# Performance work log

Hardware: AMD Instinct MI355X
Metric: run time of the kernel (lower is better)

The kernel has to match this reference:

```python
import jax, jax.numpy as jnp
import numpy as np

D = 2048  # input_size
H = 2048  # hidden_size
K = 4096  # number of children


def setup_inputs() -> dict:
    key = jax.random.key(0)
    ks = jax.random.split(key, 12)
    sD = 1.0 / np.sqrt(D)
    sH = 1.0 / np.sqrt(H)
    return {
        "input": jax.random.normal(ks[0], (D,), dtype=jnp.float32),
        "children_c": jax.random.normal(ks[1], (K, H), dtype=jnp.float32),
        "children_h": jax.random.normal(ks[2], (K, H), dtype=jnp.float32),
        "W_iou_x": jax.random.uniform(ks[3], (3 * H, D), jnp.float32, -sD, sD),
        "b_iou_x": jax.random.uniform(ks[4], (3 * H,), jnp.float32, -sD, sD),
        "W_iou_h": jax.random.uniform(ks[5], (3 * H, H), jnp.float32, -sH, sH),
        "b_iou_h": jax.random.uniform(ks[6], (3 * H,), jnp.float32, -sH, sH),
        "W_fx": jax.random.uniform(ks[7], (H, D), jnp.float32, -sD, sD),
        "b_fx": jax.random.uniform(ks[8], (H,), jnp.float32, -sD, sD),
        "W_fh": jax.random.uniform(ks[9], (H, H), jnp.float32, -sH, sH),
        "b_fh": jax.random.uniform(ks[10], (H,), jnp.float32, -sH, sH),
    }


def reference(input, children_c, children_h,
              W_iou_x, b_iou_x, W_iou_h, b_iou_h,
              W_fx, b_fx, W_fh, b_fh):
    # iou = iou_x(input) + iou_h(sum_k h_k)  -> [3H]
    h_sum = jnp.sum(children_h, axis=0)
    iou = (W_iou_x @ input + b_iou_x) + (W_iou_h @ h_sum + b_iou_h)
    i, o, u = jnp.split(iou, 3)
    i = jax.nn.sigmoid(i)
    o = jax.nn.sigmoid(o)
    u = jnp.tanh(u)
    # per-child forget gates, batched over K (original loops in Python):
    # f_k = sigmoid(f_x(input) + f_h(h_k))  -> [K, H]
    fx = W_fx @ input + b_fx                       # [H], computed once
    fh = children_h @ W_fh.T + b_fh                # [K, H] GEMM
    f = jax.nn.sigmoid(fx[None, :] + fh)           # [K, H]
    c = i * u + jnp.sum(f * children_c, axis=0)    # [H]
    h = o * jnp.tanh(c)                            # [H]
    return (o, c, h)
```

## Files before the change

### kernel.cpp

```cpp
#include <hip/hip_runtime.h>

typedef unsigned short u16;
typedef short bf16x8 __attribute__((ext_vector_type(8)));
typedef float f32x4 __attribute__((ext_vector_type(4)));

#define D_IN 2048
#define H_DIM 2048
#define K_CH 4096

__device__ __forceinline__ u16 f2bf(float f) {
  unsigned int u = __float_as_uint(f);
  u += 0x7fffu + ((u >> 16) & 1u);
  return (u16)(u >> 16);
}
__device__ __forceinline__ float sigmoidf(float x) {
  return 1.0f / (1.0f + __expf(-x));
}
__device__ __forceinline__ uint4 packrow(float4 a, float4 b) {
  uint4 w;
  w.x = (unsigned)f2bf(a.x) | ((unsigned)f2bf(a.y) << 16);
  w.y = (unsigned)f2bf(a.z) | ((unsigned)f2bf(a.w) << 16);
  w.z = (unsigned)f2bf(b.x) | ((unsigned)f2bf(b.y) << 16);
  w.w = (unsigned)f2bf(b.z) | ((unsigned)f2bf(b.w) << 16);
  return w;
}

__global__ __launch_bounds__(256) void kprep(const float* __restrict__ ch,
                                             const float* __restrict__ wfh,
                                             float* __restrict__ partials,
                                             u16* __restrict__ chb,
                                             u16* __restrict__ wfhb) {
  const int t = threadIdx.x;
  if (blockIdx.x < 256) {
    const int r0 = blockIdx.x * 16;
    float s0 = 0.f, s1 = 0.f, s2 = 0.f, s3 = 0.f;
    float s4 = 0.f, s5 = 0.f, s6 = 0.f, s7 = 0.f;
#pragma unroll
    for (int gq = 0; gq < 4; ++gq) {
      float4 a[4], b[4];
#pragma unroll
      for (int r = 0; r < 4; ++r) {
        const float4* p =
            (const float4*)(ch + (size_t)(r0 + gq * 4 + r) * H_DIM + t * 8);
        a[r] = p[0];
        b[r] = p[1];
      }
#pragma unroll
      for (int r = 0; r < 4; ++r) {
        s0 += a[r].x; s1 += a[r].y; s2 += a[r].z; s3 += a[r].w;
        s4 += b[r].x; s5 += b[r].y; s6 += b[r].z; s7 += b[r].w;
        *(uint4*)(chb + (size_t)(r0 + gq * 4 + r) * H_DIM + t * 8) =
            packrow(a[r], b[r]);
      }
    }
    float4 lo, hi;
    lo.x = s0; lo.y = s1; lo.z = s2; lo.w = s3;
    hi.x = s4; hi.y = s5; hi.z = s6; hi.w = s7;
    float* pp = partials + (size_t)blockIdx.x * H_DIM + t * 8;
    *(float4*)pp = lo;
    *(float4*)(pp + 4) = hi;
  } else {
    const size_t base = (size_t)(blockIdx.x - 256) * 16384 + t * 8;
#pragma unroll
    for (int gq = 0; gq < 2; ++gq) {
      float4 a[4], b[4];
#pragma unroll
      for (int j = 0; j < 4; ++j) {
        const float4* p = (const float4*)(wfh + base + (gq * 4 + j) * 2048);
        a[j] = p[0];
        b[j] = p[1];
      }
#pragma unroll
      for (int j = 0; j < 4; ++j)
        *(uint4*)(wfhb + base + (gq * 4 + j) * 2048) = packrow(a[j], b[j]);
    }
  }
}

__global__ __launch_bounds__(256) void kred(const float* __restrict__ partials,
                                            float* __restrict__ hsum) {
  const int c = blockIdx.x * 256 + threadIdx.x;
  float acc0 = 0.f, acc1 = 0.f, acc2 = 0.f, acc3 = 0.f;
  float acc4 = 0.f, acc5 = 0.f, acc6 = 0.f, acc7 = 0.f;
  for (int p = 0; p < 256; p += 8) {
    acc0 += partials[(size_t)(p + 0) * H_DIM + c];
    acc1 += partials[(size_t)(p + 1) * H_DIM + c];
    acc2 += partials[(size_t)(p + 2) * H_DIM + c];
    acc3 += partials[(size_t)(p + 3) * H_DIM + c];
    acc4 += partials[(size_t)(p + 4) * H_DIM + c];
    acc5 += partials[(size_t)(p + 5) * H_DIM + c];
    acc6 += partials[(size_t)(p + 6) * H_DIM + c];
    acc7 += partials[(size_t)(p + 7) * H_DIM + c];
  }
  hsum[c] = ((acc0 + acc1) + (acc2 + acc3)) + ((acc4 + acc5) + (acc6 + acc7));
}

__global__ __launch_bounds__(256) void kmatvec(
    const float* __restrict__ Wix, const float* __restrict__ bix,
    const float* __restrict__ Wih, const float* __restrict__ bih,
    const float* __restrict__ Wfx, const float* __restrict__ bfx,
    const float* __restrict__ bfh, const float* __restrict__ x,
    const float* __restrict__ hsum, float* __restrict__ iou,
    float* __restrict__ g) {
  const int wave = threadIdx.x >> 6, lane = threadIdx.x & 63;
  const int row = blockIdx.x * 4 + wave;
  float s = 0.f;
  if (row < 6144) {
    const float4* wx = (const float4*)(Wix + (size_t)row * D_IN);
    const float4* wh = (const float4*)(Wih + (size_t)row * H_DIM);
    const float4* xv = (const float4*)x;
    const float4* hv = (const float4*)hsum;
#pragma unroll
    for (int i = 0; i < 8; ++i) {
      int idx = i * 64 + lane;
      float4 a = wx[idx], b = xv[idx];
      s += a.x * b.x + a.y * b.y + a.z * b.z + a.w * b.w;
      float4 c = wh[idx], d = hv[idx];
      s += c.x * d.x + c.y * d.y + c.z * d.z + c.w * d.w;
    }
#pragma unroll
    for (int off = 32; off > 0; off >>= 1) s += __shfl_xor(s, off);
    if (lane == 0) iou[row] = s + bix[row] + bih[row];
  } else {
    const int h = row - 6144;
    const float4* w = (const float4*)(Wfx + (size_t)h * D_IN);
    const float4* xv = (const float4*)x;
#pragma unroll
    for (int i = 0; i < 8; ++i) {
      int idx = i * 64 + lane;
      float4 a = w[idx], b = xv[idx];
      s += a.x * b.x + a.y * b.y + a.z * b.z + a.w * b.w;
    }
#pragma unroll
    for (int off = 32; off > 0; off >>= 1) s += __shfl_xor(s, off);
    if (lane == 0) g[h] = s + bfx[h] + bfh[h];
  }
}

#define BM 128
#define BN 128
#define BK 32

__global__ __launch_bounds__(256) void kgemm(
    const u16* __restrict__ chb, const float* __restrict__ cc,
    const u16* __restrict__ wfhb, const float* __restrict__ g,
    float* __restrict__ accv) {
  __shared__ u16 As[BM * BK];
  __shared__ u16 Bs[BN * BK];

  const int t = threadIdx.x;
  const int wave = t >> 6, lane = t & 63;
  const int lrow = lane & 15, lquad = lane >> 4;
  const int wm = wave >> 1, wn = wave & 1;
  const int row0 = blockIdx.x * BM;
  const int col0 = blockIdx.y * BN;

  f32x4 acc[4][4] = {};

  const int stage_row = t >> 2;
  const int stage_k = (t & 3) * 8;

  for (int kb = 0; kb < D_IN / BK; ++kb) {
    __syncthreads();
    const u16* ag = chb  + (size_t)(row0 + stage_row) * H_DIM + kb * BK + stage_k;
    const u16* bg = wfhb + (size_t)(col0 + stage_row) * H_DIM + kb * BK + stage_k;
    __builtin_amdgcn_global_load_lds(
        (const __attribute__((address_space(1))) void*)ag,
        (__attribute__((address_space(3))) void*)(As + wave * 512), 16, 0, 0);
    __builtin_amdgcn_global_load_lds(
        (const __attribute__((address_space(1))) void*)(ag + (size_t)64 * H_DIM),
        (__attribute__((address_space(3))) void*)(As + 2048 + wave * 512), 16, 0, 0);
    __builtin_amdgcn_global_load_lds(
        (const __attribute__((address_space(1))) void*)bg,
        (__attribute__((address_space(3))) void*)(Bs + wave * 512), 16, 0, 0);
    __builtin_amdgcn_global_load_lds(
        (const __attribute__((address_space(1))) void*)(bg + (size_t)64 * H_DIM),
        (__attribute__((address_space(3))) void*)(Bs + 2048 + wave * 512), 16, 0, 0);
    __syncthreads();

    bf16x8 fragA[4], fragB[4];
#pragma unroll
    for (int i = 0; i < 4; ++i)
      fragA[i] = *(const bf16x8*)(As + (wm * 64 + i * 16 + lrow) * BK + lquad * 8);
#pragma unroll
    for (int i = 0; i < 4; ++i)
      fragB[i] = *(const bf16x8*)(Bs + (wn * 64 + i * 16 + lrow) * BK + lquad * 8);
#pragma unroll
    for (int mi = 0; mi < 4; ++mi)
#pragma unroll
      for (int ni = 0; ni < 4; ++ni)
        acc[mi][ni] = __builtin_amdgcn_mfma_f32_16x16x32_bf16(
            fragA[mi], fragB[ni], acc[mi][ni], 0, 0, 0);
  }

#pragma unroll
  for (int ni = 0; ni < 4; ++ni) {
    const int colg = col0 + wn * 64 + ni * 16 + lrow;
    const float gv = g[colg];
    float s = 0.f;
#pragma unroll
    for (int mi = 0; mi < 4; ++mi) {
      const int rowg = row0 + wm * 64 + mi * 16 + lquad * 4;
#pragma unroll
      for (int r = 0; r < 4; ++r) {
        float f = sigmoidf(gv + acc[mi][ni][r]);
        s += f * cc[(size_t)(rowg + r) * H_DIM + colg];
      }
    }
    s += __shfl_xor(s, 16);
    s += __shfl_xor(s, 32);
    if (lquad == 0) atomicAdd(accv + colg, s);
  }
}

__global__ __launch_bounds__(256) void kfinal(const float* __restrict__ iou,
                                              const float* __restrict__ accv,
                                              float* __restrict__ out) {
  const int h = blockIdx.x * 256 + threadIdx.x;
  float si = sigmoidf(iou[h]);
  float so = sigmoidf(iou[H_DIM + h]);
  float tu = tanhf(iou[2 * H_DIM + h]);
  float c = si * tu + accv[h];
  float hh = so * tanhf(c);
  out[h] = so;
  out[H_DIM + h] = c;
  out[2 * H_DIM + h] = hh;
}

extern "C" void kernel_launch(void* const* d_in, const int* in_sizes, int n_in,
                              void* d_out, int out_size, void* d_ws, size_t ws_size,
                              hipStream_t stream) {
  const float* x   = (const float*)d_in[0];
  const float* cc  = (const float*)d_in[1];
  const float* ch  = (const float*)d_in[2];
  const float* Wix = (const float*)d_in[3];
  const float* bix = (const float*)d_in[4];
  const float* Wih = (const float*)d_in[5];
  const float* bih = (const float*)d_in[6];
  const float* Wfx = (const float*)d_in[7];
  const float* bfx = (const float*)d_in[8];
  const float* Wfh = (const float*)d_in[9];
  const float* bfh = (const float*)d_in[10];

  float* ws   = (float*)d_ws;
  float* hsum = ws;
  float* iou  = ws + 2048;
  float* g    = ws + 8192;
  float* accv = ws + 10240;
  float* partials = ws + 12288;
  u16* chb  = (u16*)(ws + 12288 + 256 * 2048);
  u16* wfhb = chb + (size_t)K_CH * H_DIM;
  float* out = (float*)d_out;

  hipMemsetAsync(accv, 0, 2048 * sizeof(float), stream);
  kprep<<<512, 256, 0, stream>>>(ch, Wfh, partials, chb, wfhb);
  kred<<<8, 256, 0, stream>>>(partials, hsum);
  kmatvec<<<2048, 256, 0, stream>>>(Wix, bix, Wih, bih, Wfx, bfx, bfh, x, hsum, iou, g);
  kgemm<<<dim3(32, 16), 256, 0, stream>>>(chb, cc, wfhb, g, accv);
  kfinal<<<8, 256, 0, stream>>>(iou, accv, out);
}
```

Measured before the change: 292.0 us.

## Double GEMM K-tile with XOR-swizzled LDS and split prep into more blocks

The GEMM K-tile grows from 32 to 64, halving the number of barrier-separated load iterations. An XOR swizzle on the 16-byte chunk index, applied both to the global-to-LDS staging and to the fragment reads, is meant to avoid LDS bank conflicts with the wider rows. The prep kernel now has each block handle 4 rows instead of 16, launching 1536 blocks for more parallelism. In exchange the final reduction must sum 1024 partials instead of 256, which adds extra memory traffic.

```diff
diff --git a/kernel.cpp b/kernel.cpp
--- a/kernel.cpp
+++ b/kernel.cpp
@@ -31,27 +31,22 @@
                                              u16* __restrict__ chb,
                                              u16* __restrict__ wfhb) {
   const int t = threadIdx.x;
-  if (blockIdx.x < 256) {
-    const int r0 = blockIdx.x * 16;
+  if (blockIdx.x < 1024) {
+    const int r0 = blockIdx.x * 4;
+    float4 a[4], b[4];
+#pragma unroll
+    for (int r = 0; r < 4; ++r) {
+      const float4* p = (const float4*)(ch + (size_t)(r0 + r) * H_DIM + t * 8);
+      a[r] = p[0];
+      b[r] = p[1];
+    }
     float s0 = 0.f, s1 = 0.f, s2 = 0.f, s3 = 0.f;
     float s4 = 0.f, s5 = 0.f, s6 = 0.f, s7 = 0.f;
 #pragma unroll
-    for (int gq = 0; gq < 4; ++gq) {
-      float4 a[4], b[4];
-#pragma unroll
-      for (int r = 0; r < 4; ++r) {
-        const float4* p =
-            (const float4*)(ch + (size_t)(r0 + gq * 4 + r) * H_DIM + t * 8);
-        a[r] = p[0];
-        b[r] = p[1];
-      }
-#pragma unroll
-      for (int r = 0; r < 4; ++r) {
-        s0 += a[r].x; s1 += a[r].y; s2 += a[r].z; s3 += a[r].w;
-        s4 += b[r].x; s5 += b[r].y; s6 += b[r].z; s7 += b[r].w;
-        *(uint4*)(chb + (size_t)(r0 + gq * 4 + r) * H_DIM + t * 8) =
-            packrow(a[r], b[r]);
-      }
+    for (int r = 0; r < 4; ++r) {
+      s0 += a[r].x; s1 += a[r].y; s2 += a[r].z; s3 += a[r].w;
+      s4 += b[r].x; s5 += b[r].y; s6 += b[r].z; s7 += b[r].w;
+      *(uint4*)(chb + (size_t)(r0 + r) * H_DIM + t * 8) = packrow(a[r], b[r]);
     }
     float4 lo, hi;
     lo.x = s0; lo.y = s1; lo.z = s2; lo.w = s3;
@@ -60,39 +55,36 @@
     *(float4*)pp = lo;
     *(float4*)(pp + 4) = hi;
   } else {
-    const size_t base = (size_t)(blockIdx.x - 256) * 16384 + t * 8;
-#pragma unroll
-    for (int gq = 0; gq < 2; ++gq) {
-      float4 a[4], b[4];
-#pragma unroll
-      for (int j = 0; j < 4; ++j) {
-        const float4* p = (const float4*)(wfh + base + (gq * 4 + j) * 2048);
-        a[j] = p[0];
-        b[j] = p[1];
-      }
-#pragma unroll
-      for (int j = 0; j < 4; ++j)
-        *(uint4*)(wfhb + base + (gq * 4 + j) * 2048) = packrow(a[j], b[j]);
-    }
+    const size_t base = (size_t)(blockIdx.x - 1024) * 8192 + t * 8;
+    float4 a[4], b[4];
+#pragma unroll
+    for (int j = 0; j < 4; ++j) {
+      const float4* p = (const float4*)(wfh + base + j * 2048);
+      a[j] = p[0];
+      b[j] = p[1];
+    }
+#pragma unroll
+    for (int j = 0; j < 4; ++j)
+      *(uint4*)(wfhb + base + j * 2048) = packrow(a[j], b[j]);
   }
 }
 
 __global__ __launch_bounds__(256) void kred(const float* __restrict__ partials,
                                             float* __restrict__ hsum) {
   const int c = blockIdx.x * 256 + threadIdx.x;
-  float acc0 = 0.f, acc1 = 0.f, acc2 = 0.f, acc3 = 0.f;
-  float acc4 = 0.f, acc5 = 0.f, acc6 = 0.f, acc7 = 0.f;
-  for (int p = 0; p < 256; p += 8) {
-    acc0 += partials[(size_t)(p + 0) * H_DIM + c];
-    acc1 += partials[(size_t)(p + 1) * H_DIM + c];
-    acc2 += partials[(size_t)(p + 2) * H_DIM + c];
-    acc3 += partials[(size_t)(p + 3) * H_DIM + c];
-    acc4 += partials[(size_t)(p + 4) * H_DIM + c];
-    acc5 += partials[(size_t)(p + 5) * H_DIM + c];
-    acc6 += partials[(size_t)(p + 6) * H_DIM + c];
-    acc7 += partials[(size_t)(p + 7) * H_DIM + c];
-  }
-  hsum[c] = ((acc0 + acc1) + (acc2 + acc3)) + ((acc4 + acc5) + (acc6 + acc7));
+  float a0 = 0.f, a1 = 0.f, a2 = 0.f, a3 = 0.f;
+  float a4 = 0.f, a5 = 0.f, a6 = 0.f, a7 = 0.f;
+  for (int p = 0; p < 1024; p += 8) {
+    a0 += partials[(size_t)(p + 0) * H_DIM + c];
+    a1 += partials[(size_t)(p + 1) * H_DIM + c];
+    a2 += partials[(size_t)(p + 2) * H_DIM + c];
+    a3 += partials[(size_t)(p + 3) * H_DIM + c];
+    a4 += partials[(size_t)(p + 4) * H_DIM + c];
+    a5 += partials[(size_t)(p + 5) * H_DIM + c];
+    a6 += partials[(size_t)(p + 6) * H_DIM + c];
+    a7 += partials[(size_t)(p + 7) * H_DIM + c];
+  }
+  hsum[c] = ((a0 + a1) + (a2 + a3)) + ((a4 + a5) + (a6 + a7));
 }
 
 __global__ __launch_bounds__(256) void kmatvec(
@@ -139,7 +131,7 @@
 
 #define BM 128
 #define BN 128
-#define BK 32
+#define BK 64
 
 __global__ __launch_bounds__(256) void kgemm(
     const u16* __restrict__ chb, const float* __restrict__ cc,
@@ -157,40 +149,44 @@
 
   f32x4 acc[4][4] = {};
 
-  const int stage_row = t >> 2;
-  const int stage_k = (t & 3) * 8;
+  const int srow = lane >> 3;
+  const int schunk = (lane & 7) ^ srow;
+  const u16* agbase = chb  + (size_t)(row0 + wave * 32 + srow) * H_DIM + schunk * 8;
+  const u16* bgbase = wfhb + (size_t)(col0 + wave * 32 + srow) * H_DIM + schunk * 8;
 
   for (int kb = 0; kb < D_IN / BK; ++kb) {
     __syncthreads();
-    const u16* ag = chb  + (size_t)(row0 + stage_row) * H_DIM + kb * BK + stage_k;
-    const u16* bg = wfhb + (size_t)(col0 + stage_row) * H_DIM + kb * BK + stage_k;
-    __builtin_amdgcn_global_load_lds(
-        (const __attribute__((address_space(1))) void*)ag,
-        (__attribute__((address_space(3))) void*)(As + wave * 512), 16, 0, 0);
-    __builtin_amdgcn_global_load_lds(
-        (const __attribute__((address_space(1))) void*)(ag + (size_t)64 * H_DIM),
-        (__attribute__((address_space(3))) void*)(As + 2048 + wave * 512), 16, 0, 0);
-    __builtin_amdgcn_global_load_lds(
-        (const __attribute__((address_space(1))) void*)bg,
-        (__attribute__((address_space(3))) void*)(Bs + wave * 512), 16, 0, 0);
-    __builtin_amdgcn_global_load_lds(
-        (const __attribute__((address_space(1))) void*)(bg + (size_t)64 * H_DIM),
-        (__attribute__((address_space(3))) void*)(Bs + 2048 + wave * 512), 16, 0, 0);
+#pragma unroll
+    for (int i = 0; i < 4; ++i)
+      __builtin_amdgcn_global_load_lds(
+          (const __attribute__((address_space(1))) void*)(agbase + (size_t)i * 8 * H_DIM + kb * BK),
+          (__attribute__((address_space(3))) void*)(As + (wave * 32 + i * 8) * 64),
+          16, 0, 0);
+#pragma unroll
+    for (int i = 0; i < 4; ++i)
+      __builtin_amdgcn_global_load_lds(
+          (const __attribute__((address_space(1))) void*)(bgbase + (size_t)i * 8 * H_DIM + kb * BK),
+          (__attribute__((address_space(3))) void*)(Bs + (wave * 32 + i * 8) * 64),
+          16, 0, 0);
     __syncthreads();
 
-    bf16x8 fragA[4], fragB[4];
-#pragma unroll
-    for (int i = 0; i < 4; ++i)
-      fragA[i] = *(const bf16x8*)(As + (wm * 64 + i * 16 + lrow) * BK + lquad * 8);
-#pragma unroll
-    for (int i = 0; i < 4; ++i)
-      fragB[i] = *(const bf16x8*)(Bs + (wn * 64 + i * 16 + lrow) * BK + lquad * 8);
-#pragma unroll
-    for (int mi = 0; mi < 4; ++mi)
-#pragma unroll
-      for (int ni = 0; ni < 4; ++ni)
-        acc[mi][ni] = __builtin_amdgcn_mfma_f32_16x16x32_bf16(
-            fragA[mi], fragB[ni], acc[mi][ni], 0, 0, 0);
+#pragma unroll
+    for (int step = 0; step < 2; ++step) {
+      const int slot = ((step * 4 + lquad) ^ (lrow & 7)) * 8;
+      bf16x8 fa[4], fb[4];
+#pragma unroll
+      for (int i = 0; i < 4; ++i)
+        fa[i] = *(const bf16x8*)(As + (wm * 64 + i * 16 + lrow) * 64 + slot);
+#pragma unroll
+      for (int i = 0; i < 4; ++i)
+        fb[i] = *(const bf16x8*)(Bs + (wn * 64 + i * 16 + lrow) * 64 + slot);
+#pragma unroll
+      for (int mi = 0; mi < 4; ++mi)
+#pragma unroll
+        for (int ni = 0; ni < 4; ++ni)
+          acc[mi][ni] = __builtin_amdgcn_mfma_f32_16x16x32_bf16(
+              fa[mi], fb[ni], acc[mi][ni], 0, 0, 0);
+    }
   }
 
 #pragma unroll
@@ -248,12 +244,12 @@
   float* g    = ws + 8192;
   float* accv = ws + 10240;
   float* partials = ws + 12288;
-  u16* chb  = (u16*)(ws + 12288 + 256 * 2048);
+  u16* chb  = (u16*)(ws + 12288 + 1024 * 2048);
   u16* wfhb = chb + (size_t)K_CH * H_DIM;
   float* out = (float*)d_out;
 
   hipMemsetAsync(accv, 0, 2048 * sizeof(float), stream);
-  kprep<<<512, 256, 0, stream>>>(ch, Wfh, partials, chb, wfhb);
+  kprep<<<1536, 256, 0, stream>>>(ch, Wfh, partials, chb, wfhb);
   kred<<<8, 256, 0, stream>>>(partials, hsum);
   kmatvec<<<2048, 256, 0, stream>>>(Wix, bix, Wih, bih, Wfx, bfx, bfh, x, hsum, iou, g);
   kgemm<<<dim3(32, 16), 256, 0, stream>>>(chb, cc, wfhb, g, accv);
```

New measurement: 333.4 us. 14.2% more time.
